# Performance work log

Measured on AMD Instinct MI355X. Metric: run time of the kernel, lower is better.

Reference implementation:

```python
import jax, jax.numpy as jnp
import numpy as np

B, T, C = 8, 512, 1024
H, E = 16, 64          # n_head, head_dim; H*E == C
L = 2048               # cached (prefix) length in the KV cache


def setup_inputs() -> dict:
    key = jax.random.key(0)
    ks = jax.random.split(key, 6)
    scale = 0.02
    return {
        "x": jax.random.normal(ks[0], (B, T, C), jnp.float32),
        "k_cache": jax.random.normal(ks[1], (B, H, L, E), jnp.float32),
        "v_cache": jax.random.normal(ks[2], (B, H, L, E), jnp.float32),
        "Wqkv": jax.random.normal(ks[3], (C, 3 * C), jnp.float32) * scale,
        "bqkv": jnp.zeros((3 * C,), jnp.float32),
        "Wproj": jax.random.normal(ks[4], (C, C), jnp.float32) * scale,
        "bproj": jnp.zeros((C,), jnp.float32),
    }


def reference(x, k_cache, v_cache, Wqkv, bqkv, Wproj, bproj):
    qkv = x @ Wqkv + bqkv
    q, k, v = jnp.split(qkv, 3, axis=-1)

    def to_heads(t):
        return t.reshape(B, T, H, E).transpose(0, 2, 1, 3)

    q, k, v = to_heads(q), to_heads(k), to_heads(v)

    # append new k,v to the cache (kv_cache.update + get)
    k_full = jnp.concatenate([k_cache, k], axis=2)  # (B,H,L+T,E)
    v_full = jnp.concatenate([v_cache, v], axis=2)

    # manual self-attention with cache-offset causal mask: row i (global pos L+i)
    # may attend to cols j <= L+i  (bias[L:L+T, :L+T])
    att = jnp.einsum("bhte,bhse->bhts", q, k_full) * (1.0 / np.sqrt(E))
    i = jnp.arange(T)[:, None] + L
    j = jnp.arange(L + T)[None, :]
    att = jnp.where(j <= i, att, -jnp.inf)
    att = jax.nn.softmax(att, axis=-1)

    y = jnp.einsum("bhts,bhse->bhte", att, v_full)
    y = y.transpose(0, 2, 1, 3).reshape(B, T, C)
    return y @ Wproj + bproj
```

## Files before the change

kernel.cpp:

```cpp
#include <hip/hip_runtime.h>
#include <hip/hip_bf16.h>

typedef unsigned short u16;
typedef unsigned int u32;

constexpr int B_ = 8, T_ = 512, C_ = 1024, H_ = 16, E_ = 64, L_ = 2048;
constexpr int S_ = L_ + T_;

typedef __bf16 bf16x8 __attribute__((ext_vector_type(8)));
typedef float f32x4 __attribute__((ext_vector_type(4)));
typedef float f32x16 __attribute__((ext_vector_type(16)));

#define QSCALE 0.18033688011112042f


__device__ inline u16 f2bf(float f) {
  u32 u = __float_as_uint(f);
  u32 r = (u + 0x7fffu + ((u >> 16) & 1u)) >> 16;
  return (u16)r;
}

__device__ inline u32 pk2(float a, float b) {
  u32 r;
  asm("v_cvt_pk_bf16_f32 %0, %1, %2" : "=v"(r) : "v"(a), "v"(b));
  return r;
}

__device__ inline void pl32swap(u32& a, u32& b) {
  asm("v_permlane32_swap_b32 %0, %1" : "+v"(a), "+v"(b));
}

__device__ inline void gload_lds16(const u16* g, u16* l) {
  __builtin_amdgcn_global_load_lds(
      (const __attribute__((address_space(1))) u32*)g,
      (__attribute__((address_space(3))) u32*)l, 16, 0, 0);
}

__global__ __launch_bounds__(256) void convert_f32_bf16(const float* __restrict__ in,
                                                        u16* __restrict__ out) {
  const int i = blockIdx.x * 256 + threadIdx.x;
  const float4 a0 = ((const float4*)in)[i * 2];
  const float4 a1 = ((const float4*)in)[i * 2 + 1];
  uint4 p;
  p.x = pk2(a0.x, a0.y);
  p.y = pk2(a0.z, a0.w);
  p.z = pk2(a1.x, a1.y);
  p.w = pk2(a1.z, a1.w);
  ((uint4*)out)[i] = p;
}

__global__ __launch_bounds__(256) void transpose_f32_bf16(const float* __restrict__ in,
                                                          u16* __restrict__ out,
                                                          int R, int Ccols) {
  __shared__ u16 tile[64][65];
  const int r0 = blockIdx.y * 64;
  const int c0 = blockIdx.x * 64;
  const int tr = threadIdx.x >> 6;
  const int tc = threadIdx.x & 63;
#pragma unroll
  for (int i = 0; i < 16; ++i)
    tile[tr + i * 4][tc] = f2bf(in[(size_t)(r0 + tr + i * 4) * Ccols + c0 + tc]);
  __syncthreads();
#pragma unroll
  for (int i = 0; i < 16; ++i)
    out[(size_t)(c0 + tr + i * 4) * R + r0 + tc] = tile[tc][tr + i * 4];
}

__global__ __launch_bounds__(256) void prep_kv(const float* __restrict__ kc,
                                               const float* __restrict__ vc,
                                               u16* __restrict__ Km,
                                               u16* __restrict__ Vtm) {
  __shared__ u16 vt[64 * 72];
  const int s0 = (blockIdx.x & 31) * 64;
  const int bh = blockIdx.x >> 5;
  const int tid = threadIdx.x;
  const int srow = tid >> 2;
  const int eq = (tid & 3) * 16;

  {
    const float* kp = kc + ((size_t)bh * L_ + s0 + srow) * E_ + eq;
    float kv[16];
    *(float4*)(kv + 0) = *(const float4*)(kp + 0);
    *(float4*)(kv + 4) = *(const float4*)(kp + 4);
    *(float4*)(kv + 8) = *(const float4*)(kp + 8);
    *(float4*)(kv + 12) = *(const float4*)(kp + 12);
    uint4 p0, p1;
    p0.x = pk2(kv[0], kv[1]);
    p0.y = pk2(kv[2], kv[3]);
    p0.z = pk2(kv[4], kv[5]);
    p0.w = pk2(kv[6], kv[7]);
    p1.x = pk2(kv[8], kv[9]);
    p1.y = pk2(kv[10], kv[11]);
    p1.z = pk2(kv[12], kv[13]);
    p1.w = pk2(kv[14], kv[15]);
    const int sx = (srow & 7) << 3;
    u16* kd = Km + ((size_t)bh * S_ + s0 + srow) * E_;
    *(uint4*)(kd + (eq ^ sx)) = p0;
    *(uint4*)(kd + ((eq + 8) ^ sx)) = p1;
  }
  {
    const float* vp = vc + ((size_t)bh * L_ + s0 + srow) * E_ + eq;
    float vv[16];
    *(float4*)(vv + 0) = *(const float4*)(vp + 0);
    *(float4*)(vv + 4) = *(const float4*)(vp + 4);
    *(float4*)(vv + 8) = *(const float4*)(vp + 8);
    *(float4*)(vv + 12) = *(const float4*)(vp + 12);
    uint4 p0, p1;
    p0.x = pk2(vv[0], vv[1]);
    p0.y = pk2(vv[2], vv[3]);
    p0.z = pk2(vv[4], vv[5]);
    p0.w = pk2(vv[6], vv[7]);
    p1.x = pk2(vv[8], vv[9]);
    p1.y = pk2(vv[10], vv[11]);
    p1.z = pk2(vv[12], vv[13]);
    p1.w = pk2(vv[14], vv[15]);
    *(uint4*)(vt + srow * 72 + eq) = p0;
    *(uint4*)(vt + srow * 72 + eq + 8) = p1;
  }
  __syncthreads();
  {
    const int erow = tid >> 2;
    const int sq = (tid & 3) * 16;
    u16 o[16];
#pragma unroll
    for (int j = 0; j < 16; ++j) o[j] = vt[(sq + j) * 72 + erow];
    const int ex = (erow & 7) << 3;
    u16* vd = Vtm + ((size_t)bh * E_ + erow) * S_ + s0;
    *(uint4*)(vd + (sq ^ ex)) = *(uint4*)(o + 0);
    *(uint4*)(vd + ((sq + 8) ^ ex)) = *(uint4*)(o + 8);
  }
}

template <int MODE>
__global__ __launch_bounds__(256) void gemm128(const u16* __restrict__ A,
                                               const u16* __restrict__ BT,
                                               const float* __restrict__ bias,
                                               u16* __restrict__ qh,
                                               u16* __restrict__ Km,
                                               u16* __restrict__ Vtm,
                                               float* __restrict__ outf,
                                               int M, int N, int K) {
  __shared__ __align__(16) u16 As[128 * 32];
  __shared__ __align__(16) u16 Bs[128 * 32];
  const int tid = threadIdx.x;
  const int lane = tid & 63;
  const int w = tid >> 6;
  const int m0 = blockIdx.y * 128;
  const int n0 = blockIdx.x * 128;
  const int wm = (w >> 1) * 64;
  const int wn = (w & 1) * 64;
  const int fm = lane & 15;
  const int fk = (lane >> 4) * 8;

  const int srow = w * 16 + (lane >> 2);
  const int scol = (lane & 3) * 8;
  const u16* Ag = A + (size_t)(m0 + srow) * K + scol;
  const u16* Bg = BT + (size_t)(n0 + srow) * K + scol;
  u16* AsU = As + w * 512;
  u16* BsU = Bs + w * 512;

  f32x4 acc[4][4];
#pragma unroll
  for (int i = 0; i < 4; ++i)
#pragma unroll
    for (int j = 0; j < 4; ++j) acc[i][j] = f32x4{0.f, 0.f, 0.f, 0.f};

  for (int k0 = 0; k0 < K; k0 += 32) {
    gload_lds16(Ag, AsU);
    gload_lds16(Ag + (size_t)64 * K, AsU + 2048);
    gload_lds16(Bg, BsU);
    gload_lds16(Bg + (size_t)64 * K, BsU + 2048);
    Ag += 32;
    Bg += 32;
    __syncthreads();
    bf16x8 af[4], bf[4];
#pragma unroll
    for (int i = 0; i < 4; ++i)
      af[i] = *(const bf16x8*)(As + (wm + i * 16 + fm) * 32 + fk);
#pragma unroll
    for (int j = 0; j < 4; ++j)
      bf[j] = *(const bf16x8*)(Bs + (wn + j * 16 + fm) * 32 + fk);
#pragma unroll
    for (int i = 0; i < 4; ++i)
#pragma unroll
      for (int j = 0; j < 4; ++j)
        acc[i][j] = __builtin_amdgcn_mfma_f32_16x16x32_bf16(af[i], bf[j], acc[i][j], 0, 0, 0);
    __syncthreads();
  }

  const int rbase = (lane >> 4) * 4;
  const int cbase = lane & 15;
#pragma unroll
  for (int i = 0; i < 4; ++i)
#pragma unroll
    for (int j = 0; j < 4; ++j) {
      const int n = n0 + wn + j * 16 + cbase;
      const float bv = bias[n];
#pragma unroll
      for (int r = 0; r < 4; ++r) {
        const int m = m0 + wm + i * 16 + rbase + r;
        const float v = acc[i][j][r] + bv;
        if (MODE == 0) {
          const int seg = n >> 10;
          const int c = n & 1023;
          const int e = c & 63;
          const int bhh = ((m >> 9) * H_) + (c >> 6);
          const int t = m & 511;
          if (seg == 0)
            qh[((size_t)bhh * T_ + t) * E_ + e] = f2bf(v * QSCALE);
          else if (seg == 1)
            Km[((size_t)bhh * S_ + L_ + t) * E_ + (e ^ ((t & 7) << 3))] = f2bf(v);
          else
            Vtm[((size_t)bhh * E_ + e) * S_ + ((L_ + t) ^ ((e & 7) << 3))] = f2bf(v);
        } else {
          outf[(size_t)m * N + n] = v;
        }
      }
    }
}

__global__ __launch_bounds__(256, 2) void attn_v8(const u16* __restrict__ qh,
                                                  const u16* __restrict__ Km,
                                                  const u16* __restrict__ Vtm,
                                                  u16* __restrict__ y2) {
  __shared__ __align__(16) u16 Ksf[3 * 4096];
  __shared__ __align__(16) u16 Vtsf[3 * 4096];

  const int tid = threadIdx.x;
  const int lane = tid & 63;
  const int w = tid >> 6;
  const int bh = blockIdx.x & 127;
  const int qt = blockIdx.x >> 7;
  const int h = bh & (H_ - 1);
  const int b = bh >> 4;
  const int t0 = qt * 128;

  const int ln = lane & 31;
  const int hi = lane >> 5;
  const int swz = ln & 7;

  const u16* qbase = qh + ((size_t)bh * T_ + t0 + w * 32 + ln) * E_;
  bf16x8 qf[4];
#pragma unroll
  for (int et = 0; et < 4; ++et)
    qf[et] = *(const bf16x8*)(qbase + et * 16 + hi * 8);

  const int l8 = lane >> 3;
  const int u8 = lane & 7;
  const u16* kgl = Km + ((size_t)bh * S_ + w * 16 + l8) * E_ + u8 * 8;
  const u16* vgl = Vtm + ((size_t)bh * E_ + w * 16 + l8) * S_ + u8 * 8;
  const int kdst = w * 1024;

#define STAGE(cc, bi)                                                       \
  do {                                                                      \
    gload_lds16(kgl + (size_t)(cc) * 64 * E_, Ksf + (bi) * 4096 + kdst);    \
    gload_lds16(kgl + ((size_t)(cc) * 64 + 8) * E_,                         \
                Ksf + (bi) * 4096 + kdst + 512);                            \
    gload_lds16(vgl + (cc) * 64, Vtsf + (bi) * 4096 + kdst);                \
    gload_lds16(vgl + (size_t)8 * S_ + (cc) * 64,                           \
                Vtsf + (bi) * 4096 + kdst + 512);                           \
  } while (0)

  f32x16 Yt[2], lacc, zero16;
#pragma unroll
  for (int i = 0; i < 16; ++i) {
    Yt[0][i] = 0.f;
    Yt[1][i] = 0.f;
    lacc[i] = 0.f;
    zero16[i] = 0.f;
  }

  const bf16x8 ones = {(__bf16)1.f, (__bf16)1.f, (__bf16)1.f, (__bf16)1.f,
                       (__bf16)1.f, (__bf16)1.f, (__bf16)1.f, (__bf16)1.f};

  const int qmin_w = L_ + t0 + w * 32;
  const int qpos = qmin_w + ln;
  const int nchunk = (L_ + t0 + 128) >> 6;

  STAGE(0, 0);
  STAGE(1, 1);
  asm volatile("s_waitcnt vmcnt(4)" ::: "memory");
  __builtin_amdgcn_s_barrier();

  int i0 = 0, i1 = 1, i2 = 2;
  for (int c = 0; c < nchunk; ++c) {
    if (c + 2 < nchunk) STAGE(c + 2, i2);

    if ((c << 6) <= qmin_w + 31) {
      const int sbase = c << 6;
      const u16* ks = Ksf + i0 * 4096;
      const u16* vs = Vtsf + i0 * 4096;
      bf16x8 pa[4];
#pragma unroll
      for (int kb = 0; kb < 2; ++kb) {
        f32x16 s;
#pragma unroll
        for (int et = 0; et < 4; ++et) {
          const bf16x8 kf = *(const bf16x8*)(
              ks + (kb * 32 + ln) * 64 + (((et * 2 + hi) ^ swz) * 8));
          s = __builtin_amdgcn_mfma_f32_32x32x16_bf16(kf, qf[et],
                                                      et == 0 ? zero16 : s, 0, 0, 0);
        }

        if (sbase + 63 > qmin_w) {
          const int mb = sbase + kb * 32 + hi * 4;
#pragma unroll
          for (int rr = 0; rr < 16; ++rr) {
            const int keypos = mb + (rr & 3) + 8 * (rr >> 2);
            if (keypos > qpos) s[rr] = -1e30f;
          }
        }

#pragma unroll
        for (int rr = 0; rr < 16; ++rr) s[rr] = exp2f(s[rr]);

#pragma unroll
        for (int t = 0; t < 2; ++t) {
          u32 x0 = pk2(s[8 * t + 0], s[8 * t + 1]);
          u32 y0 = pk2(s[8 * t + 4], s[8 * t + 5]);
          u32 x1 = pk2(s[8 * t + 2], s[8 * t + 3]);
          u32 y1 = pk2(s[8 * t + 6], s[8 * t + 7]);
          pl32swap(x0, y0);
          pl32swap(x1, y1);
          union { u32 u[4]; bf16x8 v; } pu;
          pu.u[0] = x0;
          pu.u[1] = x1;
          pu.u[2] = y0;
          pu.u[3] = y1;
          pa[kb * 2 + t] = pu.v;
        }
      }

#pragma unroll
      for (int t = 0; t < 4; ++t)
        lacc = __builtin_amdgcn_mfma_f32_32x32x16_bf16(ones, pa[t], lacc, 0, 0, 0);

#pragma unroll
      for (int eb = 0; eb < 2; ++eb)
#pragma unroll
        for (int t = 0; t < 4; ++t) {
          const bf16x8 vf = *(const bf16x8*)(
              vs + (eb * 32 + ln) * 64 + (((t * 2 + hi) ^ swz) * 8));
          Yt[eb] = __builtin_amdgcn_mfma_f32_32x32x16_bf16(vf, pa[t], Yt[eb], 0, 0, 0);
        }
    }

    if (c + 2 < nchunk)
      asm volatile("s_waitcnt vmcnt(4)" ::: "memory");
    else if (c + 1 < nchunk)
      asm volatile("s_waitcnt vmcnt(0)" ::: "memory");
    if (c + 1 < nchunk) __builtin_amdgcn_s_barrier();

    const int tmp = i0;
    i0 = i1;
    i1 = i2;
    i2 = tmp;
  }
#undef STAGE

  const float rl = 1.f / lacc[0];
  const int t_out = t0 + w * 32 + ln;
  u16* yp = y2 + ((size_t)b * T_ + t_out) * C_ + h * E_ + hi * 4;
#pragma unroll
  for (int eb = 0; eb < 2; ++eb)
#pragma unroll
    for (int g = 0; g < 4; ++g) {
      uint2 st;
      st.x = pk2(Yt[eb][4 * g + 0] * rl, Yt[eb][4 * g + 1] * rl);
      st.y = pk2(Yt[eb][4 * g + 2] * rl, Yt[eb][4 * g + 3] * rl);
      *(uint2*)(yp + eb * 32 + g * 8) = st;
    }
}

extern "C" void kernel_launch(void* const* d_in, const int* in_sizes, int n_in,
                              void* d_out, int out_size, void* d_ws, size_t ws_size,
                              hipStream_t stream) {
  const float* x = (const float*)d_in[0];
  const float* kc = (const float*)d_in[1];
  const float* vc = (const float*)d_in[2];
  const float* Wqkv = (const float*)d_in[3];
  const float* bqkv = (const float*)d_in[4];
  const float* Wproj = (const float*)d_in[5];
  const float* bproj = (const float*)d_in[6];
  float* out = (float*)d_out;

  u16* qh = (u16*)d_ws;
  u16* y2 = qh + 4194304;
  u16* xb = y2 + 4194304;
  u16* WqT = xb + 4194304;
  u16* WpT = WqT + 3145728;
  u16* Km = WpT + 1048576;
  u16* Vtm = Km + 20971520;

  convert_f32_bf16<<<dim3(2048), 256, 0, stream>>>(x, xb);
  transpose_f32_bf16<<<dim3(48, 16), 256, 0, stream>>>(Wqkv, WqT, 1024, 3072);
  transpose_f32_bf16<<<dim3(16, 16), 256, 0, stream>>>(Wproj, WpT, 1024, 1024);
  prep_kv<<<dim3(128 * 32), 256, 0, stream>>>(kc, vc, Km, Vtm);

  gemm128<0><<<dim3(24, 32), 256, 0, stream>>>(xb, WqT, bqkv, qh, Km, Vtm, nullptr,
                                               4096, 3072, 1024);

  attn_v8<<<dim3(512), 256, 0, stream>>>(qh, Km, Vtm, y2);

  gemm128<1><<<dim3(8, 32), 256, 0, stream>>>(y2, WpT, bproj, nullptr, nullptr,
                                              nullptr, out, 4096, 1024, 1024);
}
```

Measured before the change: 335.7 us.

## Split attention KV range across two wave groups per block and reduce in LDS

The attention kernel now launches 512 threads per block: two groups of four waves each process half of the key/value chunks for the same 128 queries (split-K style). The partial outputs and row sums are combined through shared memory at the end, and one group writes the normalized result. K and V staging is also reshaped: triple-buffered K, double-buffered V, issued at different times. The aim is more waves in flight and shorter serial chunk loops per wave, at the cost of more LDS, an extra reduction step, and launch bounds that may limit registers.

```diff
diff --git a/kernel.cpp b/kernel.cpp
--- a/kernel.cpp
+++ b/kernel.cpp
@@ -219,16 +219,18 @@
     }
 }
 
-__global__ __launch_bounds__(256, 2) void attn_v8(const u16* __restrict__ qh,
+__global__ __launch_bounds__(512, 4) void attn_v9(const u16* __restrict__ qh,
                                                   const u16* __restrict__ Km,
                                                   const u16* __restrict__ Vtm,
                                                   u16* __restrict__ y2) {
-  __shared__ __align__(16) u16 Ksf[3 * 4096];
-  __shared__ __align__(16) u16 Vtsf[3 * 4096];
+  __shared__ __align__(16) u16 Ksf[6 * 4096];
+  __shared__ __align__(16) u16 Vtsf[4 * 4096];
 
   const int tid = threadIdx.x;
   const int lane = tid & 63;
   const int w = tid >> 6;
+  const int wq = w & 3;
+  const int side = w >> 2;
   const int bh = blockIdx.x & 127;
   const int qt = blockIdx.x >> 7;
   const int h = bh & (H_ - 1);
@@ -239,7 +241,7 @@
   const int hi = lane >> 5;
   const int swz = ln & 7;
 
-  const u16* qbase = qh + ((size_t)bh * T_ + t0 + w * 32 + ln) * E_;
+  const u16* qbase = qh + ((size_t)bh * T_ + t0 + wq * 32 + ln) * E_;
   bf16x8 qf[4];
 #pragma unroll
   for (int et = 0; et < 4; ++et)
@@ -247,18 +249,29 @@
 
   const int l8 = lane >> 3;
   const int u8 = lane & 7;
-  const u16* kgl = Km + ((size_t)bh * S_ + w * 16 + l8) * E_ + u8 * 8;
-  const u16* vgl = Vtm + ((size_t)bh * E_ + w * 16 + l8) * S_ + u8 * 8;
-  const int kdst = w * 1024;
-
-#define STAGE(cc, bi)                                                       \
-  do {                                                                      \
-    gload_lds16(kgl + (size_t)(cc) * 64 * E_, Ksf + (bi) * 4096 + kdst);    \
-    gload_lds16(kgl + ((size_t)(cc) * 64 + 8) * E_,                         \
-                Ksf + (bi) * 4096 + kdst + 512);                            \
-    gload_lds16(vgl + (cc) * 64, Vtsf + (bi) * 4096 + kdst);                \
-    gload_lds16(vgl + (size_t)8 * S_ + (cc) * 64,                           \
-                Vtsf + (bi) * 4096 + kdst + 512);                           \
+  const u16* kgl = Km + ((size_t)bh * S_ + wq * 16 + l8) * E_ + u8 * 8;
+  const u16* vgl = Vtm + ((size_t)bh * E_ + wq * 16 + l8) * S_ + u8 * 8;
+  const int kdst = wq * 1024;
+
+  const int qmin_w = L_ + t0 + wq * 32;
+  const int qpos = qmin_w + ln;
+  const int nchunk = (L_ + t0 + 128) >> 6;
+  const int m = nchunk >> 1;
+  const int c0 = side ? m : 0;
+
+#define STAGE_K(rr, kb)                                                        \
+  do {                                                                         \
+    gload_lds16(kgl + (size_t)(c0 + (rr)) * 64 * E_,                           \
+                Ksf + (side * 3 + (kb)) * 4096 + kdst);                        \
+    gload_lds16(kgl + ((size_t)(c0 + (rr)) * 64 + 8) * E_,                     \
+                Ksf + (side * 3 + (kb)) * 4096 + kdst + 512);                  \
+  } while (0)
+#define STAGE_V(rr, vb)                                                        \
+  do {                                                                         \
+    gload_lds16(vgl + (c0 + (rr)) * 64,                                        \
+                Vtsf + (side * 2 + (vb)) * 4096 + kdst);                       \
+    gload_lds16(vgl + (size_t)8 * S_ + (c0 + (rr)) * 64,                       \
+                Vtsf + (side * 2 + (vb)) * 4096 + kdst + 512);                 \
   } while (0)
 
   f32x16 Yt[2], lacc, zero16;
@@ -273,23 +286,22 @@
   const bf16x8 ones = {(__bf16)1.f, (__bf16)1.f, (__bf16)1.f, (__bf16)1.f,
                        (__bf16)1.f, (__bf16)1.f, (__bf16)1.f, (__bf16)1.f};
 
-  const int qmin_w = L_ + t0 + w * 32;
-  const int qpos = qmin_w + ln;
-  const int nchunk = (L_ + t0 + 128) >> 6;
-
-  STAGE(0, 0);
-  STAGE(1, 1);
-  asm volatile("s_waitcnt vmcnt(4)" ::: "memory");
+  STAGE_K(0, 0);
+  STAGE_V(0, 0);
+  STAGE_K(1, 1);
+  asm volatile("s_waitcnt vmcnt(2)" ::: "memory");
   __builtin_amdgcn_s_barrier();
 
   int i0 = 0, i1 = 1, i2 = 2;
-  for (int c = 0; c < nchunk; ++c) {
-    if (c + 2 < nchunk) STAGE(c + 2, i2);
-
+  for (int r = 0; r < m; ++r) {
+    if (r + 1 < m) STAGE_V(r + 1, (r + 1) & 1);
+    if (r + 2 < m) STAGE_K(r + 2, i2);
+
+    const int c = c0 + r;
     if ((c << 6) <= qmin_w + 31) {
       const int sbase = c << 6;
-      const u16* ks = Ksf + i0 * 4096;
-      const u16* vs = Vtsf + i0 * 4096;
+      const u16* ks = Ksf + (side * 3 + i0) * 4096;
+      const u16* vs = Vtsf + (side * 2 + (r & 1)) * 4096;
       bf16x8 pa[4];
 #pragma unroll
       for (int kb = 0; kb < 2; ++kb) {
@@ -345,31 +357,50 @@
         }
     }
 
-    if (c + 2 < nchunk)
-      asm volatile("s_waitcnt vmcnt(4)" ::: "memory");
-    else if (c + 1 < nchunk)
+    if (r + 2 < m)
+      asm volatile("s_waitcnt vmcnt(2)" ::: "memory");
+    else
       asm volatile("s_waitcnt vmcnt(0)" ::: "memory");
-    if (c + 1 < nchunk) __builtin_amdgcn_s_barrier();
+    __builtin_amdgcn_s_barrier();
 
     const int tmp = i0;
     i0 = i1;
     i1 = i2;
     i2 = tmp;
   }
-#undef STAGE
-
-  const float rl = 1.f / lacc[0];
-  const int t_out = t0 + w * 32 + ln;
-  u16* yp = y2 + ((size_t)b * T_ + t_out) * C_ + h * E_ + hi * 4;
-#pragma unroll
-  for (int eb = 0; eb < 2; ++eb)
-#pragma unroll
-    for (int g = 0; g < 4; ++g) {
-      uint2 st;
-      st.x = pk2(Yt[eb][4 * g + 0] * rl, Yt[eb][4 * g + 1] * rl);
-      st.y = pk2(Yt[eb][4 * g + 2] * rl, Yt[eb][4 * g + 3] * rl);
-      *(uint2*)(yp + eb * 32 + g * 8) = st;
-    }
+#undef STAGE_K
+#undef STAGE_V
+
+  float* red = (float*)Ksf;
+  if (side == 1) {
+    float* rp = red + ((size_t)(wq * 64 + lane)) * 33;
+#pragma unroll
+    for (int i = 0; i < 16; ++i) rp[i] = Yt[0][i];
+#pragma unroll
+    for (int i = 0; i < 16; ++i) rp[16 + i] = Yt[1][i];
+    rp[32] = lacc[0];
+  }
+  __syncthreads();
+  if (side == 0) {
+    const float* rp = red + ((size_t)(wq * 64 + lane)) * 33;
+#pragma unroll
+    for (int i = 0; i < 16; ++i) Yt[0][i] += rp[i];
+#pragma unroll
+    for (int i = 0; i < 16; ++i) Yt[1][i] += rp[16 + i];
+    const float rl = 1.f / (lacc[0] + rp[32]);
+
+    const int t_out = t0 + wq * 32 + ln;
+    u16* yp = y2 + ((size_t)b * T_ + t_out) * C_ + h * E_ + hi * 4;
+#pragma unroll
+    for (int eb = 0; eb < 2; ++eb)
+#pragma unroll
+      for (int g = 0; g < 4; ++g) {
+        uint2 st;
+        st.x = pk2(Yt[eb][4 * g + 0] * rl, Yt[eb][4 * g + 1] * rl);
+        st.y = pk2(Yt[eb][4 * g + 2] * rl, Yt[eb][4 * g + 3] * rl);
+        *(uint2*)(yp + eb * 32 + g * 8) = st;
+      }
+  }
 }
 
 extern "C" void kernel_launch(void* const* d_in, const int* in_sizes, int n_in,
@@ -400,7 +431,7 @@
   gemm128<0><<<dim3(24, 32), 256, 0, stream>>>(xb, WqT, bqkv, qh, Km, Vtm, nullptr,
                                                4096, 3072, 1024);
 
-  attn_v8<<<dim3(512), 256, 0, stream>>>(qh, Km, Vtm, y2);
+  attn_v9<<<dim3(512), 512, 0, stream>>>(qh, Km, Vtm, y2);
 
   gemm128<1><<<dim3(8, 32), 256, 0, stream>>>(y2, WpT, bproj, nullptr, nullptr,
                                               nullptr, out, 4096, 1024, 1024);
```

Result: no change. 338.2 us (+0.7%).
